# Kernel optimization log

Measured on AMD Instinct MI355X. Metric: run time of the kernel, lower is better.

## Reference

```python
import jax, jax.numpy as jnp
import numpy as np

HIDDEN = 2048
N_HEADS = 16
HEAD_DIM = HIDDEN // N_HEADS
INV_NORM = 1.0 / float(np.sqrt(HEAD_DIM))
BETA = 1.0


def setup_inputs() -> dict:
    key = jax.random.key(0)
    ks = jax.random.split(key, 12)
    B, S, H = 2, 2048, HIDDEN
    scale = 1.0 / float(np.sqrt(H))
    return {
        "hidden_states": jax.random.normal(ks[0], (B, S, H), jnp.float32),
        "residual": jax.random.normal(ks[1], (B, S, H), jnp.float32),
        "alibi": jax.random.normal(ks[2], (B * N_HEADS, 1, S), jnp.float32),
        "Wq": jax.random.normal(ks[3], (H, H), jnp.float32) * scale,
        "bq": jnp.zeros((H,), jnp.float32),
        "Wk": jax.random.normal(ks[4], (H, H), jnp.float32) * scale,
        "bk": jnp.zeros((H,), jnp.float32),
        "Wv": jax.random.normal(ks[5], (H, H), jnp.float32) * scale,
        "bv": jnp.zeros((H,), jnp.float32),
        "Wd": jax.random.normal(ks[6], (H, H), jnp.float32) * scale,
        "bd": jnp.zeros((H,), jnp.float32),
    }


def reference(hidden_states, residual, alibi, Wq, bq, Wk, bk, Wv, bv, Wd, bd):
    B, S, H = hidden_states.shape
    # separate QKV projections (nn.Linear: x @ W^T + b)
    q = hidden_states @ Wq.T + bq
    k = hidden_states @ Wk.T + bk
    v = hidden_states @ Wv.T + bv
    # [B, n_heads, S, head_dim]
    q = q.reshape(B, S, N_HEADS, HEAD_DIM).transpose(0, 2, 1, 3)
    k = k.reshape(B, S, N_HEADS, HEAD_DIM).transpose(0, 2, 1, 3)
    v = v.reshape(B, S, N_HEADS, HEAD_DIM).transpose(0, 2, 1, 3)
    # baddbmm: scores = beta * alibi + inv_norm * q @ k^T, per (batch*head)
    alibi_bh = alibi.reshape(B, N_HEADS, 1, S)  # broadcasts over query dim
    scores = BETA * alibi_bh + INV_NORM * jnp.einsum("bhqd,bhkd->bhqk", q, k)
    probs = jax.nn.softmax(scores.astype(jnp.float32), axis=-1).astype(v.dtype)
    # attention dropout: p=0.0 (identity)
    ctx = jnp.einsum("bhqk,bhkd->bhqd", probs, v)  # [B,H,S,D]
    ctx = ctx.transpose(0, 2, 1, 3).reshape(B, S, H)
    out = ctx @ Wd.T + bd
    # hidden dropout p=0.0 then residual add (dropout_add)
    return out + residual
```

## Files before the change

### kernel.cpp

```cpp
#include <hip/hip_runtime.h>

#define HID   2048
#define NHEAD 16
#define HD    128
#define SEQ   2048
#define BATCH 2
#define MROWS (BATCH*SEQ)
#define NQKV  (3*HID)
#define INV_NORM 0.08838834764831845f
#define LOG2E    1.4426950408889634f
#define SCALE_L2 (INV_NORM*LOG2E)

typedef __attribute__((ext_vector_type(8)))  __bf16 bf16x8;
typedef __attribute__((ext_vector_type(4)))  float  f32x4;
typedef __attribute__((ext_vector_type(16))) float  f32x16;

typedef __attribute__((address_space(1))) void GV;
typedef __attribute__((address_space(3))) void LV;

__device__ __forceinline__ void async16(const void* g, void* l) {
  __builtin_amdgcn_global_load_lds((const GV*)g, (LV*)l, 16, 0, 0);
}

__device__ __forceinline__ unsigned short f2bf(float f) {
  unsigned u = __builtin_bit_cast(unsigned, f);
  u += 0x7FFFu + ((u >> 16) & 1u);
  return (unsigned short)(u >> 16);
}

__device__ __forceinline__ unsigned pkbf(float a, float b) {
#if __has_builtin(__builtin_amdgcn_cvt_pk_bf16_f32)
  typedef __attribute__((ext_vector_type(2))) __bf16 bf16x2;
  bf16x2 r = __builtin_amdgcn_cvt_pk_bf16_f32(a, b);
  return __builtin_bit_cast(unsigned, r);
#else
  return (unsigned)f2bf(a) | ((unsigned)f2bf(b) << 16);
#endif
}

__device__ __forceinline__ void mfma16(f32x4& c, bf16x8 a, bf16x8 b) {
  c = __builtin_amdgcn_mfma_f32_16x16x32_bf16(a, b, c, 0, 0, 0);
}

__device__ __forceinline__ bf16x8 frag(const unsigned short* buf, int row, int chunk) {
  return *(const bf16x8*)(buf + ((row * 8 + (chunk ^ (row & 7))) << 3));
}

__global__ __launch_bounds__(256) void cvt_kernel(const float* __restrict__ src,
                                                  unsigned short* __restrict__ dst, int n) {
  int i = (blockIdx.x * 256 + threadIdx.x) * 4;
  if (i >= n) return;
  float4 v = *(const float4*)(src + i);
  ushort4 o;
  o.x = f2bf(v.x); o.y = f2bf(v.y); o.z = f2bf(v.z); o.w = f2bf(v.w);
  *(ushort4*)(dst + i) = o;
}

__global__ __launch_bounds__(256) void cvtw_kernel(const float* __restrict__ W0,
                                                   const float* __restrict__ W1,
                                                   const float* __restrict__ W2,
                                                   const float* __restrict__ W3,
                                                   unsigned short* __restrict__ dst) {
  int sel = blockIdx.y;
  const float* src = (sel == 0) ? W0 : (sel == 1) ? W1 : (sel == 2) ? W2 : W3;
  unsigned short* d = dst + (size_t)sel * HID * HID;
  int i = (blockIdx.x * 256 + threadIdx.x) * 4;
  float4 v = *(const float4*)(src + i);
  ushort4 o;
  o.x = f2bf(v.x); o.y = f2bf(v.y); o.z = f2bf(v.z); o.w = f2bf(v.w);
  *(ushort4*)(d + i) = o;
}

#define BUFU (24576)
#define BUF3 (3 * BUFU)

__global__ __launch_bounds__(512, 2) void gemm_qkv384_kernel(
    const unsigned short* __restrict__ Xb, const unsigned short* __restrict__ Wb,
    const float* __restrict__ bq, const float* __restrict__ bk,
    const float* __restrict__ bv, unsigned short* __restrict__ Cout) {
  __shared__ __align__(16) unsigned short smem[BUF3];

  const int tid  = threadIdx.x;
  const int w    = tid >> 6;
  const int lane = tid & 63;
  const int l16  = lane & 15;
  const int quad = lane >> 4;
  const int wm   = (w & 3) * 64;
  const int wn   = (w >> 2) * 64;

  const int wg = blockIdx.x;
  const int sw = (wg & 7) * 32 + (wg >> 3);
  const int m0  = (sw & 15) * 256;
  const int rn0 = (sw >> 4) * 384;

  const int sr  = tid >> 3;
  const int scs = ((tid & 7) ^ (sr & 7)) * 8;
  const unsigned short* aBase = Xb + (size_t)(m0 + sr) * HID + scs;

#define STGA(UB, RB, KT)                                              \
  async16(aBase + (size_t)(RB) * HID + (KT),                          \
          (char*)smem + (UB) * 2 + (RB) * 128 + w * 1024)
#define STGB(UB, RB, KT)                                              \
  async16(bBase + (size_t)(RB) * HID + (KT),                          \
          (char*)smem + (UB) * 2 + 32768 + (RB) * 128 + w * 1024)

#define VM6  asm volatile("s_waitcnt vmcnt(6)" ::: "memory")
#define VM0  asm volatile("s_waitcnt vmcnt(0)" ::: "memory")

#define PHASE(UB, KK, STGBLK, WAITBLK)                                         \
  {                                                                            \
    const unsigned short* Ab = smem + (UB);                                    \
    const unsigned short* Bb = Ab + 16384;                                     \
    bf16x8 ta[4], tb[4];                                                       \
    ta[0] = frag(Ab, wm + l16, (KK) * 4 + quad);                               \
    _Pragma("unroll")                                                          \
    for (int j = 0; j < 4; ++j)  tb[j] = frag(Bb, wn + j * 16 + l16, (KK) * 4 + quad); \
    _Pragma("unroll")                                                          \
    for (int ii = 1; ii < 4; ++ii) ta[ii] = frag(Ab, wm + ii * 16 + l16, (KK) * 4 + quad); \
    STGBLK;                                                                    \
    __builtin_amdgcn_s_setprio(1);                                             \
    _Pragma("unroll")                                                          \
    for (int ii = 0; ii < 4; ++ii)                                             \
      _Pragma("unroll")                                                        \
      for (int j = 0; j < 4; ++j) mfma16(acc[ii][j], ta[ii], tb[j]);           \
    __builtin_amdgcn_s_setprio(0);                                             \
    asm volatile("s_waitcnt lgkmcnt(0)" ::: "memory");                         \
    WAITBLK;                                                                   \
    __builtin_amdgcn_s_barrier();                                              \
  }

  for (int p = 0; p < 3; ++p) {
    const unsigned short* bBase = Wb + (size_t)(rn0 + p * 128 + sr) * HID + scs;

    f32x4 acc[4][4];
    const f32x4 zero = {0.f, 0.f, 0.f, 0.f};
#pragma unroll
    for (int a = 0; a < 4; ++a)
#pragma unroll
      for (int j = 0; j < 4; ++j) acc[a][j] = zero;

    STGA(0, 0, 0);  STGA(0, 64, 0);  STGA(0, 128, 0);  STGA(0, 192, 0);
    STGB(0, 0, 0);  STGB(0, 64, 0);
    STGA(BUFU, 0, 64);  STGA(BUFU, 64, 64);  STGA(BUFU, 128, 64);  STGA(BUFU, 192, 64);
    STGB(BUFU, 0, 64);  STGB(BUFU, 64, 64);
    VM6;
    __builtin_amdgcn_s_barrier();

    int kb = 0;
    for (int g = 0; g < 5; ++g) {
      PHASE(0,        0, { STGA(2*BUFU, 0, kb+128); STGA(2*BUFU, 64, kb+128); STGA(2*BUFU, 128, kb+128); }, {});
      PHASE(0,        1, { STGA(2*BUFU, 192, kb+128); STGB(2*BUFU, 0, kb+128); STGB(2*BUFU, 64, kb+128); }, VM6);
      PHASE(BUFU,     0, { STGA(0, 0, kb+192); STGA(0, 64, kb+192); STGA(0, 128, kb+192); }, {});
      PHASE(BUFU,     1, { STGA(0, 192, kb+192); STGB(0, 0, kb+192); STGB(0, 64, kb+192); }, VM6);
      PHASE(2*BUFU,   0, { STGA(BUFU, 0, kb+256); STGA(BUFU, 64, kb+256); STGA(BUFU, 128, kb+256); }, {});
      PHASE(2*BUFU,   1, { STGA(BUFU, 192, kb+256); STGB(BUFU, 0, kb+256); STGB(BUFU, 64, kb+256); }, VM6);
      PHASE(0,        0, { STGA(2*BUFU, 0, kb+320); STGA(2*BUFU, 64, kb+320); STGA(2*BUFU, 128, kb+320); }, {});
      PHASE(0,        1, { STGA(2*BUFU, 192, kb+320); STGB(2*BUFU, 0, kb+320); STGB(2*BUFU, 64, kb+320); }, VM6);
      PHASE(BUFU,     0, { STGA(0, 0, kb+384); STGA(0, 64, kb+384); STGA(0, 128, kb+384); }, {});
      PHASE(BUFU,     1, { STGA(0, 192, kb+384); STGB(0, 0, kb+384); STGB(0, 64, kb+384); }, VM6);
      PHASE(2*BUFU,   0, { STGA(BUFU, 0, kb+448); STGA(BUFU, 64, kb+448); STGA(BUFU, 128, kb+448); }, {});
      PHASE(2*BUFU,   1, { STGA(BUFU, 192, kb+448); STGB(BUFU, 0, kb+448); STGB(BUFU, 64, kb+448); }, VM6);
      kb += 384;
    }

    PHASE(0,    0, {}, {});
    PHASE(0,    1, {}, VM0);
    PHASE(BUFU, 0, {}, {});
    PHASE(BUFU, 1, {}, {});

#pragma unroll
    for (int j = 0; j < 4; ++j) {
      int ng = rn0 + p * 128 + wn + j * 16 + l16;
      float bias = (ng < HID) ? bq[ng] : (ng < 2 * HID ? bk[ng - HID] : bv[ng - 2 * HID]);
#pragma unroll
      for (int a = 0; a < 4; ++a)
#pragma unroll
        for (int r = 0; r < 4; ++r) {
          int mg = m0 + wm + a * 16 + quad * 4 + r;
          Cout[(size_t)mg * NQKV + ng] = f2bf(acc[a][j][r] + bias);
        }
    }
  }
#undef STGA
#undef STGB
#undef PHASE
#undef VM6
#undef VM0
}

__global__ __launch_bounds__(512, 2) void gemm_out384_kernel(
    const unsigned short* __restrict__ Ctx, const unsigned short* __restrict__ Wdb,
    const float* __restrict__ bd, const float* __restrict__ Res,
    float* __restrict__ Out) {
  __shared__ __align__(16) unsigned short smem[BUF3];

  const int tid  = threadIdx.x;
  const int w    = tid >> 6;
  const int lane = tid & 63;
  const int l16  = lane & 15;
  const int quad = lane >> 4;
  const int wm   = (w & 3) * 64;
  const int wn   = (w >> 2) * 64;

  const int wg = blockIdx.x;
  const int sw = (wg & 7) * 32 + (wg >> 3);
  const int m0  = (sw & 15) * 256;
  const int rn0 = (sw >> 4) * 128;

  const int sr  = tid >> 3;
  const int scs = ((tid & 7) ^ (sr & 7)) * 8;
  const unsigned short* aBase = Ctx + (size_t)(m0 + sr) * HID + scs;
  const unsigned short* bBase = Wdb + (size_t)(rn0 + sr) * HID + scs;

#define STGA(UB, RB, KT)                                              \
  async16(aBase + (size_t)(RB) * HID + (KT),                          \
          (char*)smem + (UB) * 2 + (RB) * 128 + w * 1024)
#define STGB(UB, RB, KT)                                              \
  async16(bBase + (size_t)(RB) * HID + (KT),                          \
          (char*)smem + (UB) * 2 + 32768 + (RB) * 128 + w * 1024)

#define VM6  asm volatile("s_waitcnt vmcnt(6)" ::: "memory")
#define VM0  asm volatile("s_waitcnt vmcnt(0)" ::: "memory")

#define PHASE(UB, KK, STGBLK, WAITBLK)                                         \
  {                                                                            \
    const unsigned short* Ab = smem + (UB);                                    \
    const unsigned short* Bb = Ab + 16384;                                     \
    bf16x8 ta[4], tb[4];                                                       \
    ta[0] = frag(Ab, wm + l16, (KK) * 4 + quad);                               \
    _Pragma("unroll")                                                          \
    for (int j = 0; j < 4; ++j)  tb[j] = frag(Bb, wn + j * 16 + l16, (KK) * 4 + quad); \
    _Pragma("unroll")                                                          \
    for (int ii = 1; ii < 4; ++ii) ta[ii] = frag(Ab, wm + ii * 16 + l16, (KK) * 4 + quad); \
    STGBLK;                                                                    \
    __builtin_amdgcn_s_setprio(1);                                             \
    _Pragma("unroll")                                                          \
    for (int ii = 0; ii < 4; ++ii)                                             \
      _Pragma("unroll")                                                        \
      for (int j = 0; j < 4; ++j) mfma16(acc[ii][j], ta[ii], tb[j]);           \
    __builtin_amdgcn_s_setprio(0);                                             \
    asm volatile("s_waitcnt lgkmcnt(0)" ::: "memory");                         \
    WAITBLK;                                                                   \
    __builtin_amdgcn_s_barrier();                                              \
  }

  f32x4 acc[4][4];
  const f32x4 zero = {0.f, 0.f, 0.f, 0.f};
#pragma unroll
  for (int a = 0; a < 4; ++a)
#pragma unroll
    for (int j = 0; j < 4; ++j) acc[a][j] = zero;

  STGA(0, 0, 0);  STGA(0, 64, 0);  STGA(0, 128, 0);  STGA(0, 192, 0);
  STGB(0, 0, 0);  STGB(0, 64, 0);
  STGA(BUFU, 0, 64);  STGA(BUFU, 64, 64);  STGA(BUFU, 128, 64);  STGA(BUFU, 192, 64);
  STGB(BUFU, 0, 64);  STGB(BUFU, 64, 64);
  VM6;
  __builtin_amdgcn_s_barrier();

  int kb = 0;
  for (int g = 0; g < 5; ++g) {
    PHASE(0,        0, { STGA(2*BUFU, 0, kb+128); STGA(2*BUFU, 64, kb+128); STGA(2*BUFU, 128, kb+128); }, {});
    PHASE(0,        1, { STGA(2*BUFU, 192, kb+128); STGB(2*BUFU, 0, kb+128); STGB(2*BUFU, 64, kb+128); }, VM6);
    PHASE(BUFU,     0, { STGA(0, 0, kb+192); STGA(0, 64, kb+192); STGA(0, 128, kb+192); }, {});
    PHASE(BUFU,     1, { STGA(0, 192, kb+192); STGB(0, 0, kb+192); STGB(0, 64, kb+192); }, VM6);
    PHASE(2*BUFU,   0, { STGA(BUFU, 0, kb+256); STGA(BUFU, 64, kb+256); STGA(BUFU, 128, kb+256); }, {});
    PHASE(2*BUFU,   1, { STGA(BUFU, 192, kb+256); STGB(BUFU, 0, kb+256); STGB(BUFU, 64, kb+256); }, VM6);
    PHASE(0,        0, { STGA(2*BUFU, 0, kb+320); STGA(2*BUFU, 64, kb+320); STGA(2*BUFU, 128, kb+320); }, {});
    PHASE(0,        1, { STGA(2*BUFU, 192, kb+320); STGB(2*BUFU, 0, kb+320); STGB(2*BUFU, 64, kb+320); }, VM6);
    PHASE(BUFU,     0, { STGA(0, 0, kb+384); STGA(0, 64, kb+384); STGA(0, 128, kb+384); }, {});
    PHASE(BUFU,     1, { STGA(0, 192, kb+384); STGB(0, 0, kb+384); STGB(0, 64, kb+384); }, VM6);
    PHASE(2*BUFU,   0, { STGA(BUFU, 0, kb+448); STGA(BUFU, 64, kb+448); STGA(BUFU, 128, kb+448); }, {});
    PHASE(2*BUFU,   1, { STGA(BUFU, 192, kb+448); STGB(BUFU, 0, kb+448); STGB(BUFU, 64, kb+448); }, VM6);
    kb += 384;
  }

  PHASE(0,    0, {}, {});
  PHASE(0,    1, {}, VM0);
  PHASE(BUFU, 0, {}, {});
  PHASE(BUFU, 1, {}, {});

#pragma unroll
  for (int j = 0; j < 4; ++j) {
    int ng = rn0 + wn + j * 16 + l16;
    float bias = bd[ng];
#pragma unroll
    for (int a = 0; a < 4; ++a)
#pragma unroll
      for (int r = 0; r < 4; ++r) {
        int mg = m0 + wm + a * 16 + quad * 4 + r;
        size_t off = (size_t)mg * HID + ng;
        Out[off] = acc[a][j][r] + bias + Res[off];
      }
  }
#undef STGA
#undef STGB
#undef PHASE
#undef VM6
#undef VM0
}

__global__ __launch_bounds__(256) void vtrans_kernel(const unsigned short* __restrict__ QKV,
                                                     unsigned short* __restrict__ Vt) {
  __shared__ __align__(16) unsigned short T[64][72];
  const int s0 = blockIdx.x * 64, d0 = blockIdx.y * 64, bh = blockIdx.z;
  const int b = bh >> 4, h = bh & 15;
  const int tid = threadIdx.x;
#pragma unroll
  for (int i = 0; i < 2; ++i) {
    int idx = i * 256 + tid;
    int r = idx >> 3, ch = idx & 7;
    const unsigned short* g = QKV + ((size_t)b * SEQ + s0 + r) * NQKV + 2 * HID + h * HD + d0 + ch * 8;
    *(uint4*)(&T[r][ch * 8]) = *(const uint4*)g;
  }
  __syncthreads();
#pragma unroll
  for (int i = 0; i < 2; ++i) {
    int idx = i * 256 + tid;
    int d = idx >> 3, ch = idx & 7;
    unsigned short v[8];
#pragma unroll
    for (int x = 0; x < 8; ++x) v[x] = T[ch * 8 + x][d];
    unsigned short* g = Vt + ((size_t)bh * HD + d0 + d) * SEQ + s0 + ch * 8;
    *(uint4*)g = *(const uint4*)v;
  }
}

__global__ __launch_bounds__(256, 2) void attn_kernel(
    const unsigned short* __restrict__ QKV, const unsigned short* __restrict__ Vt,
    const float* __restrict__ alibi, unsigned short* __restrict__ Ctx) {
  __shared__ __align__(16) char smem[75776];
  unsigned short* Ks   = (unsigned short*)smem;
  unsigned short* Vts0 = (unsigned short*)(smem + 16384);
  unsigned short* Vts1 = (unsigned short*)(smem + 32768);
  unsigned short* Ps   = (unsigned short*)(smem + 49152);
  float*          Alsf = (float*)(smem + 67584);
  unsigned short* Qs   = (unsigned short*)smem;

  const int tid = threadIdx.x, w = tid >> 6, lane = tid & 63;
  const int l32 = lane & 31, h = lane >> 5;
  const int q0 = blockIdx.x * 128;
  const int bh = blockIdx.y, b = bh >> 4, hh = bh & 15;
  const size_t rowbase = (size_t)b * SEQ;
  const float* ali = alibi + (size_t)bh * SEQ;
  const unsigned short* Vbh = Vt + (size_t)bh * HD * SEQ;

  {
    const unsigned short* qbase = QKV + (rowbase + q0) * NQKV + hh * HD;
#pragma unroll
    for (int i = 0; i < 8; ++i) {
      int slot = i * 256 + w * 64 + lane;
      int r = slot >> 4, c = (slot & 15) ^ (r & 15);
      async16(qbase + (size_t)r * NQKV + c * 8, (char*)Qs + (size_t)(i * 256 + w * 64) * 16);
    }
    const char* asrc = (const char*)ali;
#pragma unroll
    for (int i = 0; i < 2; ++i) {
      int slot = i * 256 + w * 64 + lane;
      async16(asrc + (size_t)slot * 16, (char*)Alsf + (size_t)(i * 256 + w * 64) * 16);
    }
  }
  __syncthreads();
  bf16x8 qf[8];
  {
    int qr = w * 32 + l32;
#pragma unroll
    for (int ks = 0; ks < 8; ++ks) {
      int c = (ks * 2 + h) ^ (qr & 15);
      qf[ks] = *(const bf16x8*)(Qs + (qr * 16 + c) * 8);
    }
  }

  f32x16 oacc[4];
  float l_acc = 0.f;
#pragma unroll
  for (int nb = 0; nb < 4; ++nb)
#pragma unroll
    for (int r = 0; r < 16; ++r) oacc[nb][r] = 0.f;

  __syncthreads();

  {
    const unsigned short* kbase = QKV + rowbase * NQKV + HID + hh * HD;
#pragma unroll
    for (int i = 0; i < 4; ++i) {
      int slot = i * 256 + w * 64 + lane;
      int r = slot >> 4, c = (slot & 15) ^ (r & 15);
      async16(kbase + (size_t)r * NQKV + c * 8, (char*)Ks + (size_t)(i * 256 + w * 64) * 16);
    }
#pragma unroll
    for (int i = 0; i < 4; ++i) {
      int slot = i * 256 + w * 64 + lane;
      int r = slot >> 3, c = (slot & 7) ^ (r & 7);
      async16(Vbh + (size_t)r * SEQ + c * 8, (char*)Vts0 + (size_t)(i * 256 + w * 64) * 16);
    }
  }
  __syncthreads();

  for (int kt = 0; kt < SEQ / 64; ++kt) {
    f32x16 sacc[2];
#pragma unroll
    for (int mb = 0; mb < 2; ++mb)
#pragma unroll
      for (int r = 0; r < 16; ++r) sacc[mb][r] = 0.f;
    __builtin_amdgcn_s_setprio(1);
#pragma unroll
    for (int ks = 0; ks < 8; ++ks) {
#pragma unroll
      for (int mb = 0; mb < 2; ++mb) {
        bf16x8 kf = *(const bf16x8*)(Ks + ((mb * 32 + l32) * 16 + ((ks * 2 + h) ^ (l32 & 15))) * 8);
        sacc[mb] = __builtin_amdgcn_mfma_f32_32x32x16_bf16(kf, qf[ks], sacc[mb], 0, 0, 0);
      }
    }
    __builtin_amdgcn_s_setprio(0);
    asm volatile("s_waitcnt lgkmcnt(0)" ::: "memory");
    __builtin_amdgcn_s_barrier();

    if (kt + 1 < SEQ / 64) {
      const unsigned short* kbase = QKV + (rowbase + (kt + 1) * 64) * NQKV + HID + hh * HD;
#pragma unroll
      for (int i = 0; i < 4; ++i) {
        int slot = i * 256 + w * 64 + lane;
        int r = slot >> 4, c = (slot & 15) ^ (r & 15);
        async16(kbase + (size_t)r * NQKV + c * 8, (char*)Ks + (size_t)(i * 256 + w * 64) * 16);
      }
      const unsigned short* vbase = Vbh + (kt + 1) * 64;
      unsigned short* vdst = ((kt + 1) & 1) ? Vts1 : Vts0;
#pragma unroll
      for (int i = 0; i < 4; ++i) {
        int slot = i * 256 + w * 64 + lane;
        int r = slot >> 3, c = (slot & 7) ^ (r & 7);
        async16(vbase + (size_t)r * SEQ + c * 8, (char*)vdst + (size_t)(i * 256 + w * 64) * 16);
      }
    }

    const int qrow = w * 32 + l32;
    const float* alsk = Alsf + kt * 64 + 4 * h;
#pragma unroll
    for (int mb = 0; mb < 2; ++mb) {
#pragma unroll
      for (int g = 0; g < 4; ++g) {
        float4 av = *(const float4*)(alsk + mb * 32 + g * 8);
        float p0 = __builtin_amdgcn_exp2f(sacc[mb][g * 4 + 0] * SCALE_L2 + av.x * LOG2E);
        float p1 = __builtin_amdgcn_exp2f(sacc[mb][g * 4 + 1] * SCALE_L2 + av.y * LOG2E);
        float p2 = __builtin_amdgcn_exp2f(sacc[mb][g * 4 + 2] * SCALE_L2 + av.z * LOG2E);
        float p3 = __builtin_amdgcn_exp2f(sacc[mb][g * 4 + 3] * SCALE_L2 + av.w * LOG2E);
        l_acc += (p0 + p1) + (p2 + p3);
        uint2 pk;
        pk.x = pkbf(p0, p1);
        pk.y = pkbf(p2, p3);
        *(uint2*)(Ps + qrow * 72 + mb * 32 + g * 8 + 4 * h) = pk;
      }
    }

    const unsigned short* vcur = (kt & 1) ? Vts1 : Vts0;
    __builtin_amdgcn_s_setprio(1);
#pragma unroll
    for (int ks2 = 0; ks2 < 4; ++ks2) {
      bf16x8 pf = *(const bf16x8*)(Ps + qrow * 72 + ks2 * 16 + h * 8);
#pragma unroll
      for (int nb = 0; nb < 4; ++nb) {
        bf16x8 vf = *(const bf16x8*)(vcur + ((nb * 32 + l32) * 8 + ((ks2 * 2 + h) ^ (l32 & 7))) * 8);
        oacc[nb] = __builtin_amdgcn_mfma_f32_32x32x16_bf16(pf, vf, oacc[nb], 0, 0, 0);
      }
    }
    __builtin_amdgcn_s_setprio(0);

    asm volatile("s_waitcnt lgkmcnt(0) vmcnt(0)" ::: "memory");
    __builtin_amdgcn_s_barrier();
  }

  float lf = l_acc + __shfl_xor(l_acc, 32, 64);
  float rinv[16];
#pragma unroll
  for (int reg = 0; reg < 16; ++reg) {
    int row = (reg & 3) + 8 * (reg >> 2) + 4 * h;
    rinv[reg] = 1.0f / __shfl(lf, row, 64);
  }

#pragma unroll
  for (int nb = 0; nb < 4; ++nb)
#pragma unroll
    for (int reg = 0; reg < 16; ++reg) {
      int row = (reg & 3) + 8 * (reg >> 2) + 4 * h;
      size_t qg = rowbase + q0 + w * 32 + row;
      Ctx[qg * HID + hh * HD + nb * 32 + l32] = f2bf(oacc[nb][reg] * rinv[reg]);
    }
}

extern "C" void kernel_launch(void* const* d_in, const int* in_sizes, int n_in,
                              void* d_out, int out_size, void* d_ws, size_t ws_size,
                              hipStream_t stream) {
  const float* hidden   = (const float*)d_in[0];
  const float* residual = (const float*)d_in[1];
  const float* alibi    = (const float*)d_in[2];
  const float* Wq = (const float*)d_in[3];
  const float* bq = (const float*)d_in[4];
  const float* Wk = (const float*)d_in[5];
  const float* bk = (const float*)d_in[6];
  const float* Wv = (const float*)d_in[7];
  const float* bv = (const float*)d_in[8];
  const float* Wd = (const float*)d_in[9];
  const float* bd = (const float*)d_in[10];
  float* out = (float*)d_out;

  unsigned short* Xb    = (unsigned short*)d_ws;
  unsigned short* Wqkvb = Xb + (size_t)MROWS * HID;
  unsigned short* Wdb   = Wqkvb + (size_t)NQKV * HID;
  unsigned short* QKVb  = Wdb + (size_t)HID * HID;
  unsigned short* Ctxb  = QKVb + (size_t)MROWS * NQKV;
  unsigned short* Vtb   = Wqkvb;

  const int nX = MROWS * HID, nW = HID * HID;
  cvt_kernel<<<nX / 4 / 256, 256, 0, stream>>>(hidden, Xb, nX);
  cvtw_kernel<<<dim3(nW / 4 / 256, 4), 256, 0, stream>>>(Wq, Wk, Wv, Wd, Wqkvb);

  gemm_qkv384_kernel<<<256, 512, 0, stream>>>(Xb, Wqkvb, bq, bk, bv, QKVb);
  vtrans_kernel<<<dim3(SEQ / 64, HD / 64, BATCH * NHEAD), 256, 0, stream>>>(QKVb, Vtb);
  attn_kernel<<<dim3(SEQ / 128, BATCH * NHEAD), 256, 0, stream>>>(QKVb, Vtb, alibi, Ctxb);
  gemm_out384_kernel<<<256, 512, 0, stream>>>(Ctxb, Wdb, bd, residual, out);
}
```

Measured before the change: 444.1 us.

## Keep softmax probabilities in registers via permlane32 swap and remap attention blocks

```diff
diff --git a/kernel.cpp b/kernel.cpp
--- a/kernel.cpp
+++ b/kernel.cpp
@@ -35,6 +35,16 @@
   return __builtin_bit_cast(unsigned, r);
 #else
   return (unsigned)f2bf(a) | ((unsigned)f2bf(b) << 16);
+#endif
+}
+
+__device__ __forceinline__ void pl32swap(unsigned &a, unsigned &b) {
+#if __has_builtin(__builtin_amdgcn_permlane32_swap)
+  typedef __attribute__((ext_vector_type(2))) unsigned u32x2;
+  u32x2 r = __builtin_amdgcn_permlane32_swap(a, b, false, false);
+  a = r[0]; b = r[1];
+#else
+  asm volatile("v_permlane32_swap_b32 %0, %1" : "+v"(a), "+v"(b));
 #endif
 }
 
@@ -329,18 +339,20 @@
 __global__ __launch_bounds__(256, 2) void attn_kernel(
     const unsigned short* __restrict__ QKV, const unsigned short* __restrict__ Vt,
     const float* __restrict__ alibi, unsigned short* __restrict__ Ctx) {
-  __shared__ __align__(16) char smem[75776];
+  __shared__ __align__(16) char smem[57344];
   unsigned short* Ks   = (unsigned short*)smem;
   unsigned short* Vts0 = (unsigned short*)(smem + 16384);
   unsigned short* Vts1 = (unsigned short*)(smem + 32768);
-  unsigned short* Ps   = (unsigned short*)(smem + 49152);
-  float*          Alsf = (float*)(smem + 67584);
+  float*          Alsf = (float*)(smem + 49152);
   unsigned short* Qs   = (unsigned short*)smem;
 
   const int tid = threadIdx.x, w = tid >> 6, lane = tid & 63;
   const int l32 = lane & 31, h = lane >> 5;
-  const int q0 = blockIdx.x * 128;
-  const int bh = blockIdx.y, b = bh >> 4, hh = bh & 15;
+  const int bid = blockIdx.x;
+  const int t  = bid >> 3;
+  const int q0 = (t & 15) * 128;
+  const int bh = (bid & 7) + 8 * (t >> 4);
+  const int b = bh >> 4, hh = bh & 15;
   const size_t rowbase = (size_t)b * SEQ;
   const float* ali = alibi + (size_t)bh * SEQ;
   const unsigned short* Vbh = Vt + (size_t)bh * HD * SEQ;
@@ -434,30 +446,37 @@
       }
     }
 
-    const int qrow = w * 32 + l32;
     const float* alsk = Alsf + kt * 64 + 4 * h;
+    bf16x8 pfr[4];
 #pragma unroll
     for (int mb = 0; mb < 2; ++mb) {
+      float p[16];
 #pragma unroll
       for (int g = 0; g < 4; ++g) {
         float4 av = *(const float4*)(alsk + mb * 32 + g * 8);
-        float p0 = __builtin_amdgcn_exp2f(sacc[mb][g * 4 + 0] * SCALE_L2 + av.x * LOG2E);
-        float p1 = __builtin_amdgcn_exp2f(sacc[mb][g * 4 + 1] * SCALE_L2 + av.y * LOG2E);
-        float p2 = __builtin_amdgcn_exp2f(sacc[mb][g * 4 + 2] * SCALE_L2 + av.z * LOG2E);
-        float p3 = __builtin_amdgcn_exp2f(sacc[mb][g * 4 + 3] * SCALE_L2 + av.w * LOG2E);
-        l_acc += (p0 + p1) + (p2 + p3);
-        uint2 pk;
-        pk.x = pkbf(p0, p1);
-        pk.y = pkbf(p2, p3);
-        *(uint2*)(Ps + qrow * 72 + mb * 32 + g * 8 + 4 * h) = pk;
+        p[g * 4 + 0] = __builtin_amdgcn_exp2f(sacc[mb][g * 4 + 0] * SCALE_L2 + av.x * LOG2E);
+        p[g * 4 + 1] = __builtin_amdgcn_exp2f(sacc[mb][g * 4 + 1] * SCALE_L2 + av.y * LOG2E);
+        p[g * 4 + 2] = __builtin_amdgcn_exp2f(sacc[mb][g * 4 + 2] * SCALE_L2 + av.z * LOG2E);
+        p[g * 4 + 3] = __builtin_amdgcn_exp2f(sacc[mb][g * 4 + 3] * SCALE_L2 + av.w * LOG2E);
+        l_acc += (p[g * 4 + 0] + p[g * 4 + 1]) + (p[g * 4 + 2] + p[g * 4 + 3]);
       }
+      unsigned c0 = pkbf(p[0],  p[1]),  c1 = pkbf(p[2],  p[3]);
+      unsigned c2 = pkbf(p[4],  p[5]),  c3 = pkbf(p[6],  p[7]);
+      unsigned c4 = pkbf(p[8],  p[9]),  c5 = pkbf(p[10], p[11]);
+      unsigned c6 = pkbf(p[12], p[13]), c7 = pkbf(p[14], p[15]);
+      pl32swap(c0, c2);  pl32swap(c1, c3);
+      pl32swap(c4, c6);  pl32swap(c5, c7);
+      uint4 f0; f0.x = c0; f0.y = c1; f0.z = c2; f0.w = c3;
+      uint4 f1; f1.x = c4; f1.y = c5; f1.z = c6; f1.w = c7;
+      pfr[mb * 2 + 0] = __builtin_bit_cast(bf16x8, f0);
+      pfr[mb * 2 + 1] = __builtin_bit_cast(bf16x8, f1);
     }
 
     const unsigned short* vcur = (kt & 1) ? Vts1 : Vts0;
     __builtin_amdgcn_s_setprio(1);
 #pragma unroll
     for (int ks2 = 0; ks2 < 4; ++ks2) {
-      bf16x8 pf = *(const bf16x8*)(Ps + qrow * 72 + ks2 * 16 + h * 8);
+      bf16x8 pf = pfr[ks2];
 #pragma unroll
       for (int nb = 0; nb < 4; ++nb) {
         bf16x8 vf = *(const bf16x8*)(vcur + ((nb * 32 + l32) * 8 + ((ks2 * 2 + h) ^ (l32 & 7))) * 8);
@@ -517,6 +536,6 @@
 
   gemm_qkv384_kernel<<<256, 512, 0, stream>>>(Xb, Wqkvb, bq, bk, bv, QKVb);
   vtrans_kernel<<<dim3(SEQ / 64, HD / 64, BATCH * NHEAD), 256, 0, stream>>>(QKVb, Vtb);
-  attn_kernel<<<dim3(SEQ / 128, BATCH * NHEAD), 256, 0, stream>>>(QKVb, Vtb, alibi, Ctxb);
+  attn_kernel<<<512, 256, 0, stream>>>(QKVb, Vtb, alibi, Ctxb);
   gemm_out384_kernel<<<256, 512, 0, stream>>>(Ctxb, Wdb, bd, residual, out);
 }
```

Result: no change. 439.0 us (-1.1%).
